# Performance work log

Measured on AMD Instinct MI355X. Metric: run time of the kernel, lower is better.

The kernel has to match this reference:

```python
import jax, jax.numpy as jnp
import numpy as np

NEG_SLOPE = 0.2  # PyG GATConv default leaky_relu slope


def gat_conv(h_in, src, dst, W, a_src, a_dst, b, N):
    # h_in: [N, Fin]; src/dst: [E] (self-loops already appended)
    h = h_in @ W                      # [N, Fout]
    alpha_src = h @ a_src             # [N]
    alpha_dst = h @ a_dst             # [N]
    e = jax.nn.leaky_relu(alpha_src[src] + alpha_dst[dst], NEG_SLOPE)  # [E]
    # segment softmax over incoming edges of each destination node
    m = jax.ops.segment_max(e, dst, num_segments=N)
    m = jnp.where(jnp.isfinite(m), m, 0.0)
    p = jnp.exp(e - m[dst])
    denom = jax.ops.segment_sum(p, dst, num_segments=N)
    alpha = p / jnp.maximum(denom[dst], 1e-16)
    out = jax.ops.segment_sum(alpha[:, None] * h[src], dst, num_segments=N)
    return out + b


def setup_inputs() -> dict:
    key = jax.random.key(0)
    ks = jax.random.split(key, 16)
    N, E, V, D, H, C, G = 100000, 1600000, 128, 50, 16, 10, 512
    x = jax.random.normal(ks[0], (N, V), dtype=jnp.float32)
    edge_index = jax.random.randint(ks[1], (2, E), 0, N, dtype=jnp.int32)
    batch = jnp.sort(jax.random.randint(ks[2], (N,), 0, G, dtype=jnp.int32))
    s = lambda fan: 1.0 / np.sqrt(fan)
    return {
        "x": x, "edge_index": edge_index, "batch": batch,
        "embedding": jax.random.normal(ks[3], (V, D), dtype=jnp.float32),
        "W1": jax.random.normal(ks[4], (D, H), dtype=jnp.float32) * s(D),
        "a_src1": jax.random.normal(ks[5], (H,), dtype=jnp.float32) * s(H),
        "a_dst1": jax.random.normal(ks[6], (H,), dtype=jnp.float32) * s(H),
        "b1": jnp.zeros((H,), dtype=jnp.float32),
        "W2": jax.random.normal(ks[7], (H, H), dtype=jnp.float32) * s(H),
        "a_src2": jax.random.normal(ks[8], (H,), dtype=jnp.float32) * s(H),
        "a_dst2": jax.random.normal(ks[9], (H,), dtype=jnp.float32) * s(H),
        "b2": jnp.zeros((H,), dtype=jnp.float32),
        "W3": jax.random.normal(ks[10], (H, C), dtype=jnp.float32) * s(H),
        "a_src3": jax.random.normal(ks[11], (C,), dtype=jnp.float32) * s(C),
        "a_dst3": jax.random.normal(ks[12], (C,), dtype=jnp.float32) * s(C),
        "b3": jnp.zeros((C,), dtype=jnp.float32),
    }


def reference(x, edge_index, batch, embedding, W1, a_src1, a_dst1, b1,
              W2, a_src2, a_dst2, b2, W3, a_src3, a_dst3, b3):
    N = x.shape[0]
    G = 512  # num graphs
    # embedding lookup via argmax over one-hot-ish features
    idx = jnp.argmax(x, axis=1)
    h = embedding[idx]                               # [N, 50]
    # add self-loops once (PyG GATConv default)
    loops = jnp.arange(N, dtype=edge_index.dtype)
    src = jnp.concatenate([edge_index[0], loops])
    dst = jnp.concatenate([edge_index[1], loops])
    h = jax.nn.relu(gat_conv(h, src, dst, W1, a_src1, a_dst1, b1, N))
    # dropout: eval mode -> identity
    h = jax.nn.relu(gat_conv(h, src, dst, W2, a_src2, a_dst2, b2, N))
    h = gat_conv(h, src, dst, W3, a_src3, a_dst3, b3, N)  # [N, C]
    # global mean pool over graphs
    sums = jax.ops.segment_sum(h, batch, num_segments=G)
    cnts = jax.ops.segment_sum(jnp.ones((N,), h.dtype), batch, num_segments=G)
    pooled = sums / jnp.maximum(cnts, 1.0)[:, None]
    return jax.nn.softmax(pooled, axis=1)
```

## Files before the change

kernel.cpp:

```cpp
#include <hip/hip_runtime.h>
#include <math.h>

#define NEG_SLOPE 0.2f
#define NBUK_MAX 2048

__global__ void k_argmax(const float* __restrict__ x, int* __restrict__ idx, int N, int V) {
    int node = (blockIdx.x * blockDim.x + threadIdx.x) >> 5;
    int lane = threadIdx.x & 31;
    if (node >= N) return;
    const float4* row = (const float4*)(x + (long long)node * V);
    float bv = -INFINITY;
    int bi = 0x7fffffff;
    int nq = V >> 2;
    for (int q = lane; q < nq; q += 32) {
        float4 v = row[q];
        int base = q << 2;
        if (v.x > bv || (v.x == bv && base     < bi)) { bv = v.x; bi = base;     }
        if (v.y > bv || (v.y == bv && base + 1 < bi)) { bv = v.y; bi = base + 1; }
        if (v.z > bv || (v.z == bv && base + 2 < bi)) { bv = v.z; bi = base + 2; }
        if (v.w > bv || (v.w == bv && base + 3 < bi)) { bv = v.w; bi = base + 3; }
    }
    for (int off = 16; off > 0; off >>= 1) {
        float ov = __shfl_down(bv, off, 32);
        int   oi = __shfl_down(bi, off, 32);
        if (ov > bv || (ov == bv && oi < bi)) { bv = ov; bi = oi; }
    }
    if (lane == 0) idx[node] = bi;
}

template <int FIN, int FOUT, bool GATHER>
__global__ void k_transform(const float* __restrict__ h_in, const int* __restrict__ idx,
                            const float* __restrict__ W,
                            const float* __restrict__ a_src, const float* __restrict__ a_dst,
                            _Float16* __restrict__ h_t, float* __restrict__ asrc,
                            float* __restrict__ adst, int N) {
    __shared__ float sW[FIN * FOUT];
    __shared__ float sa[FOUT], sd[FOUT];
    for (int i = threadIdx.x; i < FIN * FOUT; i += blockDim.x) sW[i] = W[i];
    if (threadIdx.x < FOUT) { sa[threadIdx.x] = a_src[threadIdx.x]; sd[threadIdx.x] = a_dst[threadIdx.x]; }
    __syncthreads();
    int n = blockIdx.x * blockDim.x + threadIdx.x;
    if (n >= N) return;
    float acc[FOUT];
#pragma unroll
    for (int f = 0; f < FOUT; f++) acc[f] = 0.f;
    const float* hr = GATHER ? (h_in + (long long)idx[n] * FIN)
                             : (h_in + (long long)n * FIN);
    for (int k = 0; k < FIN; k++) {
        float v = hr[k];
#pragma unroll
        for (int f = 0; f < FOUT; f++) acc[f] += v * sW[k * FOUT + f];
    }
    float s1 = 0.f, s2 = 0.f;
    _Float16 hh[16];
#pragma unroll
    for (int f = 0; f < 16; f++) hh[f] = (_Float16)0.f;
#pragma unroll
    for (int f = 0; f < FOUT; f++) {
        hh[f] = (_Float16)acc[f];
        s1 += acc[f] * sa[f];
        s2 += acc[f] * sd[f];
    }
    uint4* dst = (uint4*)(h_t + (long long)n * 16);
    dst[0] = ((uint4*)hh)[0];
    dst[1] = ((uint4*)hh)[1];
    asrc[n] = s1;
    adst[n] = s2;
}

template <int B2>
__global__ void __launch_bounds__(1024)
k_histB(const int* __restrict__ edst, int E, int* __restrict__ histT, int NBUK) {
    __shared__ int sh[NBUK_MAX];
    int t = threadIdx.x, b = blockIdx.x;
    for (int k = t; k < NBUK; k += 1024) sh[k] = 0;
    __syncthreads();
    long long ebeg = (long long)b * E / B2, eend = (long long)(b + 1) * E / B2;
    for (long long i = ebeg + t; i < eend; i += 1024)
        atomicAdd(&sh[edst[i] >> 6], 1);
    __syncthreads();
    for (int k = t; k < NBUK; k += 1024) histT[(long long)k * B2 + b] = sh[k];
}

__global__ void k_scan1(const int* __restrict__ vals, int* __restrict__ excl,
                        int* __restrict__ bsums, int M) {
    __shared__ int s[256];
    int i = blockIdx.x * 256 + threadIdx.x;
    int v = (i < M) ? vals[i] : 0;
    s[threadIdx.x] = v;
    __syncthreads();
    for (int off = 1; off < 256; off <<= 1) {
        int a = (threadIdx.x >= (unsigned)off) ? s[threadIdx.x - off] : 0;
        __syncthreads();
        s[threadIdx.x] += a;
        __syncthreads();
    }
    if (i < M) excl[i] = s[threadIdx.x] - v;
    if (threadIdx.x == 255) bsums[blockIdx.x] = s[255];
}

__global__ void k_scan2(int* __restrict__ bsums, int nb) {
    __shared__ int s[2048];
    int i = threadIdx.x;
    int v0 = (i < nb) ? bsums[i] : 0;
    int v1 = (i + 1024 < nb) ? bsums[i + 1024] : 0;
    s[i] = v0;
    s[i + 1024] = v1;
    __syncthreads();
    for (int off = 1; off < 2048; off <<= 1) {
        int a0 = (i >= off) ? s[i - off] : 0;
        int a1 = (i + 1024 >= off) ? s[i + 1024 - off] : 0;
        __syncthreads();
        s[i] += a0;
        s[i + 1024] += a1;
        __syncthreads();
    }
    if (i < nb) bsums[i] = s[i] - v0;
    if (i + 1024 < nb) bsums[i + 1024] = s[i + 1024] - v1;
}

__global__ void k_scan3(const int* __restrict__ excl, const int* __restrict__ bsums,
                        int* __restrict__ soff, int M) {
    int i = blockIdx.x * 256 + threadIdx.x;
    if (i < M) soff[i] = excl[i] + bsums[i >> 8];
}

template <int B2>
__global__ void __launch_bounds__(1024)
k_scatB(const int* __restrict__ esrc, const int* __restrict__ edst, int E,
        const int* __restrict__ soff, int* __restrict__ tmp, int NBUK) {
    __shared__ int cur[NBUK_MAX];
    int t = threadIdx.x, b = blockIdx.x;
    for (int k = t; k < NBUK; k += 1024) cur[k] = soff[(long long)k * B2 + b];
    __syncthreads();
    long long ebeg = (long long)b * E / B2, eend = (long long)(b + 1) * E / B2;
    for (long long i = ebeg + t; i < eend; i += 1024) {
        int d = edst[i];
        int pos = atomicAdd(&cur[d >> 6], 1);
        tmp[pos] = ((d & 63) << 18) | esrc[i];
    }
}

template <int B2>
__global__ void __launch_bounds__(256)
k_binB(const int* __restrict__ soff, const int* __restrict__ tmp,
       int* __restrict__ rowptr, int* __restrict__ csr_src, int N, int NBUK, int E) {
    __shared__ int cnt[64];
    __shared__ int cur[64];
    int t = threadIdx.x, b = blockIdx.x;
    int t0 = soff[(long long)b * B2];
    int t1 = (b + 1 < NBUK) ? soff[(long long)(b + 1) * B2] : E;
    if (t < 64) cnt[t] = 0;
    __syncthreads();
    for (int i = t0 + t; i < t1; i += 256) atomicAdd(&cnt[tmp[i] >> 18], 1);
    __syncthreads();
    if (t < 64) {
        int v = cnt[t];
        int incl = v;
        for (int off = 1; off < 64; off <<= 1) {
            int u = __shfl_up(incl, off, 64);
            if (t >= off) incl += u;
        }
        int base = t0 + incl - v;
        int d = (b << 6) + t;
        if (d < N) rowptr[d] = base;
        cur[t] = base;
        if (d == N - 1) rowptr[N] = E;
    }
    __syncthreads();
    for (int i = t0 + t; i < t1; i += 256) {
        int p = tmp[i];
        int pos = atomicAdd(&cur[p >> 18], 1);
        csr_src[pos] = p & 0x3FFFF;
    }
}

template <int FOUT, bool BIAS, bool RELU>
__global__ void k_gat_dst(const int* __restrict__ rowptr, const int* __restrict__ csr_src,
                          const float* __restrict__ asrc, const float* __restrict__ adst,
                          const _Float16* __restrict__ h_t, const float* __restrict__ b,
                          float* __restrict__ out, int N) {
    int grp  = (blockIdx.x * blockDim.x + threadIdx.x) >> 4;
    int lane = threadIdx.x & 15;
    if (grp >= N) return;
    int d = grp;
    int r0 = rowptr[d], r1 = rowptr[d + 1];
    float ad = adst[d];
    constexpr bool FULL = (FOUT == 16);
    const bool active = FULL || lane < FOUT;

    float e0 = asrc[d] + ad;
    e0 = (e0 >= 0.f) ? e0 : NEG_SLOPE * e0;
    float p0 = __expf(e0);
    float acc  = p0 * (float)h_t[(long long)d * 16 + lane];
    float psum = (lane == 0) ? p0 : 0.f;

    for (int j = r0; j < r1; j += 16) {
        int myj = j + lane;
        bool valid = myj < r1;
        int s = valid ? csr_src[myj] : d;
        float a = asrc[s];
        float e = a + ad;
        e = (e >= 0.f) ? e : NEG_SLOPE * e;
        float p = valid ? __expf(e) : 0.f;
        psum += p;
#pragma unroll
        for (int k = 0; k < 16; k++) {
            float pk = __shfl(p, k, 16);
            int   sk = __shfl(s, k, 16);
            acc += pk * (float)h_t[(long long)sk * 16 + lane];
        }
    }
    for (int off = 8; off > 0; off >>= 1) psum += __shfl_xor(psum, off, 16);

    if (active) {
        float v = acc / fmaxf(psum, 1e-16f);
        if (BIAS) v += b[lane];
        if (RELU) v = fmaxf(v, 0.f);
        out[(long long)d * FOUT + lane] = v;
    }
}

__global__ void k_pool(const float* __restrict__ h3, const int* __restrict__ batch,
                       const float* __restrict__ b3, float* __restrict__ out, int N, int C) {
    int g = blockIdx.x;
    int lo = 0, hi = N;
    while (lo < hi) { int mid = (lo + hi) >> 1; if (batch[mid] < g) lo = mid + 1; else hi = mid; }
    int start = lo;
    hi = N;
    while (lo < hi) { int mid = (lo + hi) >> 1; if (batch[mid] < g + 1) lo = mid + 1; else hi = mid; }
    int end = lo;

    float sum[16];
    for (int f = 0; f < C; f++) sum[f] = 0.f;
    for (int n = start + threadIdx.x; n < end; n += blockDim.x) {
        const float* r = h3 + (long long)n * C;
        for (int f = 0; f < C; f++) sum[f] += r[f];
    }
    __shared__ float red[256 * 16];
    for (int f = 0; f < C; f++) red[threadIdx.x * 16 + f] = sum[f];
    __syncthreads();
    for (int str = blockDim.x / 2; str > 0; str >>= 1) {
        if ((int)threadIdx.x < str)
            for (int f = 0; f < C; f++) red[threadIdx.x * 16 + f] += red[(threadIdx.x + str) * 16 + f];
        __syncthreads();
    }
    if (threadIdx.x == 0) {
        float cnt = fmaxf((float)(end - start), 1.f);
        float vals[16];
        float mx = -INFINITY;
        for (int f = 0; f < C; f++) { vals[f] = red[f] / cnt + b3[f]; mx = fmaxf(mx, vals[f]); }
        float se = 0.f;
        for (int f = 0; f < C; f++) { vals[f] = __expf(vals[f] - mx); se += vals[f]; }
        for (int f = 0; f < C; f++) out[(long long)g * C + f] = vals[f] / se;
    }
}

extern "C" void kernel_launch(void* const* d_in, const int* in_sizes, int n_in,
                              void* d_out, int out_size, void* d_ws, size_t ws_size,
                              hipStream_t stream) {
    const float* x    = (const float*)d_in[0];
    const int*   eidx = (const int*)d_in[1];
    const int*   batch= (const int*)d_in[2];
    const float* emb  = (const float*)d_in[3];
    const float* W1   = (const float*)d_in[4];
    const float* as1  = (const float*)d_in[5];
    const float* ad1  = (const float*)d_in[6];
    const float* b1   = (const float*)d_in[7];
    const float* W2   = (const float*)d_in[8];
    const float* as2  = (const float*)d_in[9];
    const float* ad2  = (const float*)d_in[10];
    const float* b2   = (const float*)d_in[11];
    const float* W3   = (const float*)d_in[12];
    const float* as3  = (const float*)d_in[13];
    const float* ad3  = (const float*)d_in[14];
    const float* b3   = (const float*)d_in[15];

    const int H = in_sizes[5];
    const int C = in_sizes[13];
    const int D = in_sizes[4] / H;
    const int V = in_sizes[3] / D;
    const int N = in_sizes[0] / V;
    const int E = in_sizes[1] / 2;
    const int G = out_size / C;
    const int* esrc = eidx;
    const int* edst = eidx + E;
    const int NBUK = (N + 63) >> 6;
    constexpr int B2 = 256;
    const int M = NBUK * B2;

    char* w = (char*)d_ws;
    auto carve = [&](size_t bytes) {
        char* p = w;
        w += (bytes + 255) & ~(size_t)255;
        return p;
    };
    float*     asrc    = (float*)carve((size_t)N * 4);
    float*     adst    = (float*)carve((size_t)N * 4);
    int*       idx     = (int*)carve((size_t)N * 4);
    int*       rowptr  = (int*)carve((size_t)(N + 1) * 4);
    int*       csr_src = (int*)carve((size_t)E * 4);
    int*       histT   = (int*)carve((size_t)M * 4);
    int*       sexcl   = (int*)carve((size_t)M * 4);
    int*       soff    = (int*)carve((size_t)M * 4);
    int*       bsums   = (int*)carve(2048 * 4);
    _Float16*  hT      = (_Float16*)carve((size_t)N * 16 * 2);
    char*  zone = w;
    float* X0 = (float*)zone;
    float* X1 = (float*)(zone + (((size_t)N * H * 4 + 255) & ~(size_t)255));
    int*   tmp = (int*)zone;
    (void)ws_size; (void)n_in;

    const int BT = 256;
    dim3 blk(BT);
    int gN   = (N + BT - 1) / BT;
    int gArg = (N * 32 + BT - 1) / BT;
    int gGat = (N * 16 + BT - 1) / BT;
    int nb2  = (M + 255) / 256;

    k_histB<B2><<<B2, dim3(1024), 0, stream>>>(edst, E, histT, NBUK);
    k_scan1<<<nb2, blk, 0, stream>>>(histT, sexcl, bsums, M);
    k_scan2<<<1, 1024, 0, stream>>>(bsums, nb2);
    k_scan3<<<nb2, blk, 0, stream>>>(sexcl, bsums, soff, M);
    k_scatB<B2><<<B2, dim3(1024), 0, stream>>>(esrc, edst, E, soff, tmp, NBUK);
    k_binB<B2><<<NBUK, blk, 0, stream>>>(soff, tmp, rowptr, csr_src, N, NBUK, E);

    k_argmax<<<gArg, blk, 0, stream>>>(x, idx, N, V);

    k_transform<50, 16, true><<<gN, blk, 0, stream>>>(emb, idx, W1, as1, ad1, hT, asrc, adst, N);
    k_gat_dst<16, true, true><<<gGat, blk, 0, stream>>>(rowptr, csr_src, asrc, adst, hT, b1, X0, N);

    k_transform<16, 16, false><<<gN, blk, 0, stream>>>(X0, nullptr, W2, as2, ad2, hT, asrc, adst, N);
    k_gat_dst<16, true, true><<<gGat, blk, 0, stream>>>(rowptr, csr_src, asrc, adst, hT, b2, X1, N);

    k_transform<16, 10, false><<<gN, blk, 0, stream>>>(X1, nullptr, W3, as3, ad3, hT, asrc, adst, N);
    k_gat_dst<10, false, false><<<gGat, blk, 0, stream>>>(rowptr, csr_src, asrc, adst, hT, nullptr, X0, N);

    k_pool<<<G, blk, 0, stream>>>(X0, batch, b3, (float*)d_out, N, C);
}
```

Measured before the change: 275.4 us.

## Fuse argmax with first transform and next-layer transforms into GAT aggregation

```diff
diff --git a/kernel.cpp b/kernel.cpp
--- a/kernel.cpp
+++ b/kernel.cpp
@@ -4,15 +4,26 @@
 #define NEG_SLOPE 0.2f
 #define NBUK_MAX 2048
 
-__global__ void k_argmax(const float* __restrict__ x, int* __restrict__ idx, int N, int V) {
-    int node = (blockIdx.x * blockDim.x + threadIdx.x) >> 5;
-    int lane = threadIdx.x & 31;
-    if (node >= N) return;
-    const float4* row = (const float4*)(x + (long long)node * V);
+template <int FIN, int FOUT>
+__global__ void k_embed_tr(const float* __restrict__ x, const float* __restrict__ emb,
+                           const float* __restrict__ W, const float* __restrict__ a_src,
+                           const float* __restrict__ a_dst,
+                           _Float16* __restrict__ h_t, float* __restrict__ asrc,
+                           float* __restrict__ adst, int N, int V) {
+    __shared__ float sW[FIN * FOUT];
+    __shared__ float sa[FOUT], sd[FOUT];
+    for (int i = threadIdx.x; i < FIN * FOUT; i += blockDim.x) sW[i] = W[i];
+    if (threadIdx.x < FOUT) { sa[threadIdx.x] = a_src[threadIdx.x]; sd[threadIdx.x] = a_dst[threadIdx.x]; }
+    __syncthreads();
+    int grp  = (blockIdx.x * blockDim.x + threadIdx.x) >> 4;
+    int lane = threadIdx.x & 15;
+    if (grp >= N) return;
+
+    const float4* row = (const float4*)(x + (long long)grp * V);
     float bv = -INFINITY;
     int bi = 0x7fffffff;
     int nq = V >> 2;
-    for (int q = lane; q < nq; q += 32) {
+    for (int q = lane; q < nq; q += 16) {
         float4 v = row[q];
         int base = q << 2;
         if (v.x > bv || (v.x == bv && base     < bi)) { bv = v.x; bi = base;     }
@@ -20,52 +31,24 @@
         if (v.z > bv || (v.z == bv && base + 2 < bi)) { bv = v.z; bi = base + 2; }
         if (v.w > bv || (v.w == bv && base + 3 < bi)) { bv = v.w; bi = base + 3; }
     }
-    for (int off = 16; off > 0; off >>= 1) {
-        float ov = __shfl_down(bv, off, 32);
-        int   oi = __shfl_down(bi, off, 32);
+    for (int off = 8; off > 0; off >>= 1) {
+        float ov = __shfl_down(bv, off, 16);
+        int   oi = __shfl_down(bi, off, 16);
         if (ov > bv || (ov == bv && oi < bi)) { bv = ov; bi = oi; }
     }
-    if (lane == 0) idx[node] = bi;
-}
-
-template <int FIN, int FOUT, bool GATHER>
-__global__ void k_transform(const float* __restrict__ h_in, const int* __restrict__ idx,
-                            const float* __restrict__ W,
-                            const float* __restrict__ a_src, const float* __restrict__ a_dst,
-                            _Float16* __restrict__ h_t, float* __restrict__ asrc,
-                            float* __restrict__ adst, int N) {
-    __shared__ float sW[FIN * FOUT];
-    __shared__ float sa[FOUT], sd[FOUT];
-    for (int i = threadIdx.x; i < FIN * FOUT; i += blockDim.x) sW[i] = W[i];
-    if (threadIdx.x < FOUT) { sa[threadIdx.x] = a_src[threadIdx.x]; sd[threadIdx.x] = a_dst[threadIdx.x]; }
-    __syncthreads();
-    int n = blockIdx.x * blockDim.x + threadIdx.x;
-    if (n >= N) return;
-    float acc[FOUT];
-#pragma unroll
-    for (int f = 0; f < FOUT; f++) acc[f] = 0.f;
-    const float* hr = GATHER ? (h_in + (long long)idx[n] * FIN)
-                             : (h_in + (long long)n * FIN);
-    for (int k = 0; k < FIN; k++) {
-        float v = hr[k];
-#pragma unroll
-        for (int f = 0; f < FOUT; f++) acc[f] += v * sW[k * FOUT + f];
-    }
-    float s1 = 0.f, s2 = 0.f;
-    _Float16 hh[16];
-#pragma unroll
-    for (int f = 0; f < 16; f++) hh[f] = (_Float16)0.f;
-#pragma unroll
-    for (int f = 0; f < FOUT; f++) {
-        hh[f] = (_Float16)acc[f];
-        s1 += acc[f] * sa[f];
-        s2 += acc[f] * sd[f];
-    }
-    uint4* dst = (uint4*)(h_t + (long long)n * 16);
-    dst[0] = ((uint4*)hh)[0];
-    dst[1] = ((uint4*)hh)[1];
-    asrc[n] = s1;
-    adst[n] = s2;
+    bi = __shfl(bi, 0, 16);
+
+    const float* hr = emb + (long long)bi * FIN;
+    float acc = 0.f;
+    for (int k = 0; k < FIN; k++) acc += hr[k] * sW[k * FOUT + lane];
+
+    float c1 = acc * sa[lane], c2 = acc * sd[lane];
+    for (int off = 8; off > 0; off >>= 1) {
+        c1 += __shfl_xor(c1, off, 16);
+        c2 += __shfl_xor(c2, off, 16);
+    }
+    h_t[(long long)grp * 16 + lane] = (_Float16)acc;
+    if (lane == 0) { asrc[grp] = c1; adst[grp] = c2; }
 }
 
 template <int B2>
@@ -175,19 +158,27 @@
     }
 }
 
-template <int FOUT, bool BIAS, bool RELU>
-__global__ void k_gat_dst(const int* __restrict__ rowptr, const int* __restrict__ csr_src,
-                          const float* __restrict__ asrc, const float* __restrict__ adst,
-                          const _Float16* __restrict__ h_t, const float* __restrict__ b,
-                          float* __restrict__ out, int N) {
+template <int FN>
+__global__ void k_gat_ft(const int* __restrict__ rowptr, const int* __restrict__ csr_src,
+                         const float* __restrict__ asrc, const float* __restrict__ adst,
+                         const _Float16* __restrict__ h_t, const float* __restrict__ bias,
+                         const float* __restrict__ Wn, const float* __restrict__ an_src,
+                         const float* __restrict__ an_dst,
+                         _Float16* __restrict__ h_next, float* __restrict__ asrc_n,
+                         float* __restrict__ adst_n, int N) {
+    __shared__ float sW[16 * FN];
+    __shared__ float sa[FN], sd[FN], sb[16];
+    for (int i = threadIdx.x; i < 16 * FN; i += blockDim.x) sW[i] = Wn[i];
+    if (threadIdx.x < FN) { sa[threadIdx.x] = an_src[threadIdx.x]; sd[threadIdx.x] = an_dst[threadIdx.x]; }
+    if (threadIdx.x < 16) sb[threadIdx.x] = bias[threadIdx.x];
+    __syncthreads();
+
     int grp  = (blockIdx.x * blockDim.x + threadIdx.x) >> 4;
     int lane = threadIdx.x & 15;
     if (grp >= N) return;
     int d = grp;
     int r0 = rowptr[d], r1 = rowptr[d + 1];
     float ad = adst[d];
-    constexpr bool FULL = (FOUT == 16);
-    const bool active = FULL || lane < FOUT;
 
     float e0 = asrc[d] + ad;
     e0 = (e0 >= 0.f) ? e0 : NEG_SLOPE * e0;
@@ -213,12 +204,62 @@
     }
     for (int off = 8; off > 0; off >>= 1) psum += __shfl_xor(psum, off, 16);
 
-    if (active) {
-        float v = acc / fmaxf(psum, 1e-16f);
-        if (BIAS) v += b[lane];
-        if (RELU) v = fmaxf(v, 0.f);
-        out[(long long)d * FOUT + lane] = v;
-    }
+    float v = acc / fmaxf(psum, 1e-16f) + sb[lane];
+    v = fmaxf(v, 0.f);
+
+    float acc2 = 0.f;
+#pragma unroll
+    for (int k = 0; k < 16; k++) {
+        float vk = __shfl(v, k, 16);
+        if (lane < FN) acc2 += vk * sW[k * FN + lane];
+    }
+    float c1 = (lane < FN) ? acc2 * sa[lane] : 0.f;
+    float c2 = (lane < FN) ? acc2 * sd[lane] : 0.f;
+    for (int off = 8; off > 0; off >>= 1) {
+        c1 += __shfl_xor(c1, off, 16);
+        c2 += __shfl_xor(c2, off, 16);
+    }
+    h_next[(long long)d * 16 + lane] = (_Float16)((lane < FN) ? acc2 : 0.f);
+    if (lane == 0) { asrc_n[d] = c1; adst_n[d] = c2; }
+}
+
+template <int FOUT>
+__global__ void k_gat_dst(const int* __restrict__ rowptr, const int* __restrict__ csr_src,
+                          const float* __restrict__ asrc, const float* __restrict__ adst,
+                          const _Float16* __restrict__ h_t, float* __restrict__ out, int N) {
+    int grp  = (blockIdx.x * blockDim.x + threadIdx.x) >> 4;
+    int lane = threadIdx.x & 15;
+    if (grp >= N) return;
+    int d = grp;
+    int r0 = rowptr[d], r1 = rowptr[d + 1];
+    float ad = adst[d];
+
+    float e0 = asrc[d] + ad;
+    e0 = (e0 >= 0.f) ? e0 : NEG_SLOPE * e0;
+    float p0 = __expf(e0);
+    float acc  = p0 * (float)h_t[(long long)d * 16 + lane];
+    float psum = (lane == 0) ? p0 : 0.f;
+
+    for (int j = r0; j < r1; j += 16) {
+        int myj = j + lane;
+        bool valid = myj < r1;
+        int s = valid ? csr_src[myj] : d;
+        float a = asrc[s];
+        float e = a + ad;
+        e = (e >= 0.f) ? e : NEG_SLOPE * e;
+        float p = valid ? __expf(e) : 0.f;
+        psum += p;
+#pragma unroll
+        for (int k = 0; k < 16; k++) {
+            float pk = __shfl(p, k, 16);
+            int   sk = __shfl(s, k, 16);
+            acc += pk * (float)h_t[(long long)sk * 16 + lane];
+        }
+    }
+    for (int off = 8; off > 0; off >>= 1) psum += __shfl_xor(psum, off, 16);
+
+    if (lane < FOUT)
+        out[(long long)d * FOUT + lane] = acc / fmaxf(psum, 1e-16f);
 }
 
 __global__ void k_pool(const float* __restrict__ h3, const int* __restrict__ batch,
@@ -295,26 +336,26 @@
         w += (bytes + 255) & ~(size_t)255;
         return p;
     };
-    float*     asrc    = (float*)carve((size_t)N * 4);
-    float*     adst    = (float*)carve((size_t)N * 4);
-    int*       idx     = (int*)carve((size_t)N * 4);
+    float*     as_a    = (float*)carve((size_t)N * 4);
+    float*     ad_a    = (float*)carve((size_t)N * 4);
+    float*     as_b    = (float*)carve((size_t)N * 4);
+    float*     ad_b    = (float*)carve((size_t)N * 4);
     int*       rowptr  = (int*)carve((size_t)(N + 1) * 4);
     int*       csr_src = (int*)carve((size_t)E * 4);
     int*       histT   = (int*)carve((size_t)M * 4);
     int*       sexcl   = (int*)carve((size_t)M * 4);
     int*       soff    = (int*)carve((size_t)M * 4);
     int*       bsums   = (int*)carve(2048 * 4);
-    _Float16*  hT      = (_Float16*)carve((size_t)N * 16 * 2);
-    char*  zone = w;
-    float* X0 = (float*)zone;
-    float* X1 = (float*)(zone + (((size_t)N * H * 4 + 255) & ~(size_t)255));
+    _Float16*  hTa     = (_Float16*)carve((size_t)N * 16 * 2);
+    _Float16*  hTb     = (_Float16*)carve((size_t)N * 16 * 2);
+    size_t zone_bytes = ((size_t)E * 4 > (size_t)N * C * 4) ? (size_t)E * 4 : (size_t)N * C * 4;
+    char*  zone = carve(zone_bytes);
+    float* X0  = (float*)zone;
     int*   tmp = (int*)zone;
     (void)ws_size; (void)n_in;
 
     const int BT = 256;
     dim3 blk(BT);
-    int gN   = (N + BT - 1) / BT;
-    int gArg = (N * 32 + BT - 1) / BT;
     int gGat = (N * 16 + BT - 1) / BT;
     int nb2  = (M + 255) / 256;
 
@@ -325,16 +366,15 @@
     k_scatB<B2><<<B2, dim3(1024), 0, stream>>>(esrc, edst, E, soff, tmp, NBUK);
     k_binB<B2><<<NBUK, blk, 0, stream>>>(soff, tmp, rowptr, csr_src, N, NBUK, E);
 
-    k_argmax<<<gArg, blk, 0, stream>>>(x, idx, N, V);
-
-    k_transform<50, 16, true><<<gN, blk, 0, stream>>>(emb, idx, W1, as1, ad1, hT, asrc, adst, N);
-    k_gat_dst<16, true, true><<<gGat, blk, 0, stream>>>(rowptr, csr_src, asrc, adst, hT, b1, X0, N);
-
-    k_transform<16, 16, false><<<gN, blk, 0, stream>>>(X0, nullptr, W2, as2, ad2, hT, asrc, adst, N);
-    k_gat_dst<16, true, true><<<gGat, blk, 0, stream>>>(rowptr, csr_src, asrc, adst, hT, b2, X1, N);
-
-    k_transform<16, 10, false><<<gN, blk, 0, stream>>>(X1, nullptr, W3, as3, ad3, hT, asrc, adst, N);
-    k_gat_dst<10, false, false><<<gGat, blk, 0, stream>>>(rowptr, csr_src, asrc, adst, hT, nullptr, X0, N);
+    k_embed_tr<50, 16><<<gGat, blk, 0, stream>>>(x, emb, W1, as1, ad1, hTa, as_a, ad_a, N, V);
+
+    k_gat_ft<16><<<gGat, blk, 0, stream>>>(rowptr, csr_src, as_a, ad_a, hTa, b1,
+                                           W2, as2, ad2, hTb, as_b, ad_b, N);
+
+    k_gat_ft<10><<<gGat, blk, 0, stream>>>(rowptr, csr_src, as_b, ad_b, hTb, b2,
+                                           W3, as3, ad3, hTa, as_a, ad_a, N);
+
+    k_gat_dst<10><<<gGat, blk, 0, stream>>>(rowptr, csr_src, as_a, ad_a, hTa, X0, N);
 
     k_pool<<<G, blk, 0, stream>>>(X0, batch, b3, (float*)d_out, N, C);
 }
```

Measured after the change: 280.9 us. Within noise of the previous version (+2.0%).
